# Optimization experiments

Measured on AMD Instinct MI355X. Metric: run time of the kernel, lower is better.

Reference implementation:

```python
import jax, jax.numpy as jnp
import numpy as np

N = 100_000          # nodes
E = 3_200_000        # train edges (avg degree 32)
E_TEST = 500_000     # pos/neg test edges each
F_IN, F_HID, F_OUT = 256, 16, 64


def setup_inputs() -> dict:
    key = jax.random.key(0)
    ks = jax.random.split(key, 7)
    x = jax.random.normal(ks[0], (N, F_IN), jnp.float32)
    train_edge_index = jax.random.randint(ks[1], (2, E), 0, N, dtype=jnp.int32)
    test_pos_edge_index = jax.random.randint(ks[2], (2, E_TEST), 0, N, dtype=jnp.int32)
    test_neg_edge_index = jax.random.randint(ks[3], (2, E_TEST), 0, N, dtype=jnp.int32)
    W1 = jax.random.normal(ks[4], (F_IN, F_HID), jnp.float32) / np.float32(np.sqrt(F_IN))
    b1 = jnp.zeros((F_HID,), jnp.float32)
    W2 = jax.random.normal(ks[5], (F_HID, F_OUT), jnp.float32) / np.float32(np.sqrt(F_HID))
    b2 = jnp.zeros((F_OUT,), jnp.float32)
    return dict(x=x, train_edge_index=train_edge_index,
                test_pos_edge_index=test_pos_edge_index,
                test_neg_edge_index=test_neg_edge_index,
                W1=W1, b1=b1, W2=W2, b2=b2)


def gcn_conv(x, edge_index, W, b, n):
    """PyG GCNConv: x' = D^-1/2 (A+I) D^-1/2 (x W) + b (self-loops added)."""
    h = x @ W                                  # project first (PyG order)
    loop = jnp.arange(n, dtype=edge_index.dtype)
    src = jnp.concatenate([edge_index[0], loop])
    dst = jnp.concatenate([edge_index[1], loop])
    deg = jax.ops.segment_sum(jnp.ones_like(dst, dtype=h.dtype), dst, num_segments=n)
    dinv = jnp.where(deg > 0, jax.lax.rsqrt(deg), 0.0)
    norm = dinv[src] * dinv[dst]               # per-edge symmetric norm
    msg = h[src] * norm[:, None]               # gather + scale
    out = jax.ops.segment_sum(msg, dst, num_segments=n)  # scatter-add
    return out + b


def reference(x, train_edge_index, test_pos_edge_index, test_neg_edge_index,
              W1, b1, W2, b2):
    n = x.shape[0]
    z = gcn_conv(x, train_edge_index, W1, b1, n)
    z = jax.nn.relu(z)
    z = gcn_conv(z, train_edge_index, W2, b2, n)
    edge_index = jnp.concatenate([test_pos_edge_index, test_neg_edge_index], axis=-1)
    logits = jnp.sum(z[edge_index[0]] * z[edge_index[1]], axis=-1)
    return logits
```

## Files before the change

### kernel.cpp

```cpp
#include <hip/hip_runtime.h>
#include <hip/hip_fp16.h>


#define NB_SHIFT 8
#define CAP   9728
#define CHUNK 8192

__global__ void seedprep_kernel(int* __restrict__ gtail, int nb1,
                                const float* __restrict__ W2, const float* __restrict__ b2,
                                float* __restrict__ mw) {
    int t = threadIdx.x;
    for (int i = t; i < nb1; i += 256) gtail[i] = i * CAP;
    int r = t >> 4, cc = t & 15;
    float s = 0.0f;
    for (int j = 0; j < 64; ++j) s += W2[r * 64 + j] * W2[cc * 64 + j];
    mw[t] = s;
    if (t < 16) {
        float w = 0.0f;
        for (int j = 0; j < 64; ++j) w += W2[t * 64 + j] * b2[j];
        mw[256 + t] = w;
    }
    if (t == 0) {
        float bbv = 0.0f;
        for (int j = 0; j < 64; ++j) bbv += b2[j] * b2[j];
        mw[272] = bbv;
    }
}

__global__ void __launch_bounds__(512)
passA1_kernel(const int* __restrict__ src, const int* __restrict__ dst, int E,
              int* __restrict__ gtail, unsigned* __restrict__ tmp, int nb1) {
    __shared__ int h[512];
    __shared__ int loff[512];
    __shared__ int cur[512];
    __shared__ int base[512];
    __shared__ unsigned srec[CHUNK];
    __shared__ unsigned short sbkt[CHUNK];
    int t = threadIdx.x;
    int c0 = blockIdx.x * CHUNK;
    int ce = min(CHUNK, E - c0);

    h[t] = 0;
    __syncthreads();
    for (int i = t; i < ce; i += 512)
        atomicAdd(&h[dst[c0 + i] >> NB_SHIFT], 1);
    __syncthreads();
    int cnt = h[t];
    loff[t] = cnt;
    __syncthreads();
    for (int off = 1; off < 512; off <<= 1) {
        int v = loff[t];
        int a = (t >= off) ? loff[t - off] : 0;
        __syncthreads();
        loff[t] = v + a;
        __syncthreads();
    }
    int excl = loff[t] - cnt;
    if (t < nb1) base[t] = atomicAdd(&gtail[t], cnt);
    loff[t] = excl;
    cur[t]  = excl;
    __syncthreads();
    for (int i = t; i < ce; i += 512) {
        int d = dst[c0 + i];
        int s = src[c0 + i];
        int b = d >> NB_SHIFT;
        int p = atomicAdd(&cur[b], 1);
        srec[p] = (unsigned)s | ((unsigned)(d & 255) << 20);
        sbkt[p] = (unsigned short)b;
    }
    __syncthreads();
    for (int i = t; i < ce; i += 512) {
        int b = sbkt[i];
        tmp[base[b] + (i - loff[b])] = srec[i];
    }
}

__global__ void __launch_bounds__(512)
fill2_kernel(const int* __restrict__ gtail, const unsigned* __restrict__ tmp,
             int* __restrict__ eidx, int* __restrict__ rowptr,
             int* __restrict__ counts, float* __restrict__ dinv, int n) {
    __shared__ int hh[256];
    __shared__ int sc[256];
    __shared__ int cur[256];
    __shared__ int sout[CAP];
    int b = blockIdx.x;
    int t = threadIdx.x;
    int beg = b * CAP;
    int cnt_total = gtail[b] - beg;

    if (t < 256) hh[t] = 0;
    __syncthreads();
    for (int i = t; i < cnt_total; i += 512)
        atomicAdd(&hh[tmp[beg + i] >> 20], 1);
    __syncthreads();
    if (t < 256) sc[t] = hh[t];
    __syncthreads();
    for (int off = 1; off < 256; off <<= 1) {
        int v = 0, a = 0;
        if (t < 256) { v = sc[t]; a = (t >= off) ? sc[t - off] : 0; }
        __syncthreads();
        if (t < 256) sc[t] = v + a;
        __syncthreads();
    }
    if (t < 256) {
        int ex = sc[t] - hh[t];
        cur[t] = ex;
        int v = (b << NB_SHIFT) + t;
        if (v < n) {
            rowptr[v] = beg + ex;
            counts[v] = hh[t];
            dinv[v]   = rsqrtf((float)hh[t] + 1.0f);
        }
    }
    __syncthreads();
    for (int i = t; i < cnt_total; i += 512) {
        unsigned r = tmp[beg + i];
        int p = atomicAdd(&cur[r >> 20], 1);
        sout[p] = (int)(r & 0xFFFFF);
    }
    __syncthreads();
    for (int i = t; i < cnt_total; i += 512)
        eidx[beg + i] = sout[i];
}

__global__ void __launch_bounds__(64)
gemm1_kernel(const float* __restrict__ x, const float* __restrict__ W1,
             const float* __restrict__ dinv, __half* __restrict__ hs, int n) {
    int row = blockIdx.x * 64 + threadIdx.x;
    if (row >= n) return;
    const float4* x4 = (const float4*)(x + (size_t)row * 256);
    const float4* W14 = (const float4*)W1;
    float4 a0 = {0,0,0,0}, a1 = {0,0,0,0}, a2 = {0,0,0,0}, a3 = {0,0,0,0};
    float4 buf[8];
    #pragma unroll
    for (int j = 0; j < 8; ++j) buf[j] = x4[j];
    for (int k8 = 0; k8 < 8; ++k8) {
        float4 cur[8];
        #pragma unroll
        for (int j = 0; j < 8; ++j) cur[j] = buf[j];
        if (k8 < 7) {
            #pragma unroll
            for (int j = 0; j < 8; ++j) buf[j] = x4[(k8 + 1) * 8 + j];
        }
        #pragma unroll
        for (int jj = 0; jj < 8; ++jj) {
            float4 xv = cur[jj];
            int k4 = k8 * 8 + jj;
            #pragma unroll
            for (int j = 0; j < 4; ++j) {
                float xk = (j == 0) ? xv.x : (j == 1) ? xv.y : (j == 2) ? xv.z : xv.w;
                int k = (k4 << 2) + j;
                float4 w0 = W14[k * 4 + 0];
                float4 w1 = W14[k * 4 + 1];
                float4 w2 = W14[k * 4 + 2];
                float4 w3 = W14[k * 4 + 3];
                a0.x += xk * w0.x; a0.y += xk * w0.y; a0.z += xk * w0.z; a0.w += xk * w0.w;
                a1.x += xk * w1.x; a1.y += xk * w1.y; a1.z += xk * w1.z; a1.w += xk * w1.w;
                a2.x += xk * w2.x; a2.y += xk * w2.y; a2.z += xk * w2.z; a2.w += xk * w2.w;
                a3.x += xk * w3.x; a3.y += xk * w3.y; a3.z += xk * w3.z; a3.w += xk * w3.w;
            }
        }
    }
    float di = dinv[row];
    union { __half2 h2[8]; uint4 u4[2]; } pk;
    pk.h2[0] = __floats2half2_rn(a0.x * di, a0.y * di);
    pk.h2[1] = __floats2half2_rn(a0.z * di, a0.w * di);
    pk.h2[2] = __floats2half2_rn(a1.x * di, a1.y * di);
    pk.h2[3] = __floats2half2_rn(a1.z * di, a1.w * di);
    pk.h2[4] = __floats2half2_rn(a2.x * di, a2.y * di);
    pk.h2[5] = __floats2half2_rn(a2.z * di, a2.w * di);
    pk.h2[6] = __floats2half2_rn(a3.x * di, a3.y * di);
    pk.h2[7] = __floats2half2_rn(a3.z * di, a3.w * di);
    uint4* o = (uint4*)(hs + (size_t)row * 16);
    o[0] = pk.u4[0];
    o[1] = pk.u4[1];
}

__global__ void agg1_kernel(const int* __restrict__ rowptr, const int* __restrict__ counts,
                            const int* __restrict__ eidx, const __half* __restrict__ hsh,
                            const float* __restrict__ dinv, const float* __restrict__ b1,
                            float4* __restrict__ gs4, int n) {
    const uint2* h2p = (const uint2*)hsh;
    int t = blockIdx.x * blockDim.x + threadIdx.x;
    int v = t >> 3;
    if (v >= n) return;
    int q = t & 3, hh = (t >> 2) & 1;
    int start = rowptr[v], cnt = counts[v];
    float4 s = {0, 0, 0, 0};
    int i = hh;
    for (; i + 6 < cnt; i += 8) {
        int s0 = eidx[start + i];
        int s1 = eidx[start + i + 2];
        int s2 = eidx[start + i + 4];
        int s3 = eidx[start + i + 6];
        uint2 r0 = h2p[(size_t)s0 * 4 + q];
        uint2 r1 = h2p[(size_t)s1 * 4 + q];
        uint2 r2 = h2p[(size_t)s2 * 4 + q];
        uint2 r3 = h2p[(size_t)s3 * 4 + q];
        float2 f0a = __half22float2(*(__half2*)&r0.x), f0b = __half22float2(*(__half2*)&r0.y);
        float2 f1a = __half22float2(*(__half2*)&r1.x), f1b = __half22float2(*(__half2*)&r1.y);
        float2 f2a = __half22float2(*(__half2*)&r2.x), f2b = __half22float2(*(__half2*)&r2.y);
        float2 f3a = __half22float2(*(__half2*)&r3.x), f3b = __half22float2(*(__half2*)&r3.y);
        s.x += f0a.x + f1a.x + f2a.x + f3a.x;
        s.y += f0a.y + f1a.y + f2a.y + f3a.y;
        s.z += f0b.x + f1b.x + f2b.x + f3b.x;
        s.w += f0b.y + f1b.y + f2b.y + f3b.y;
    }
    for (; i < cnt; i += 2) {
        uint2 r0 = h2p[(size_t)eidx[start + i] * 4 + q];
        float2 fa = __half22float2(*(__half2*)&r0.x), fb = __half22float2(*(__half2*)&r0.y);
        s.x += fa.x; s.y += fa.y; s.z += fb.x; s.w += fb.y;
    }
    s.x += __shfl_xor(s.x, 4);
    s.y += __shfl_xor(s.y, 4);
    s.z += __shfl_xor(s.z, 4);
    s.w += __shfl_xor(s.w, 4);
    if (hh == 0) {
        float di = dinv[v];
        uint2 rv = h2p[(size_t)v * 4 + q];
        float2 ha = __half22float2(*(__half2*)&rv.x), hb = __half22float2(*(__half2*)&rv.y);
        float4 b = ((const float4*)b1)[q];
        float4 z;
        z.x = fmaxf(di * (s.x + ha.x) + b.x, 0.0f) * di;
        z.y = fmaxf(di * (s.y + ha.y) + b.y, 0.0f) * di;
        z.z = fmaxf(di * (s.z + hb.x) + b.z, 0.0f) * di;
        z.w = fmaxf(di * (s.w + hb.y) + b.w, 0.0f) * di;
        gs4[(size_t)v * 4 + q] = z;
    }
}

__global__ void agg2y_kernel(const int* __restrict__ rowptr, const int* __restrict__ counts,
                             const int* __restrict__ eidx, const float4* __restrict__ gs4,
                             const float* __restrict__ dinv, const float* __restrict__ mw,
                             float4* __restrict__ u4, float* __restrict__ y,
                             float* __restrict__ c, int n) {
    __shared__ float su[32 * 16];
    __shared__ float sM[256];
    __shared__ float sw[16];
    int t = threadIdx.x;
    sM[t] = mw[t];
    if (t < 16) sw[t] = mw[256 + t];

    int j = t >> 3, q = t & 3, hh = (t >> 2) & 1;
    int v = blockIdx.x * 32 + j;
    if (v < n) {
        int start = rowptr[v], cnt = counts[v];
        float4 s = {0, 0, 0, 0};
        int i = hh;
        for (; i + 6 < cnt; i += 8) {
            int s0 = eidx[start + i];
            int s1 = eidx[start + i + 2];
            int s2 = eidx[start + i + 4];
            int s3 = eidx[start + i + 6];
            float4 g0 = gs4[(size_t)s0 * 4 + q];
            float4 g1 = gs4[(size_t)s1 * 4 + q];
            float4 g2 = gs4[(size_t)s2 * 4 + q];
            float4 g3 = gs4[(size_t)s3 * 4 + q];
            s.x += g0.x + g1.x + g2.x + g3.x;
            s.y += g0.y + g1.y + g2.y + g3.y;
            s.z += g0.z + g1.z + g2.z + g3.z;
            s.w += g0.w + g1.w + g2.w + g3.w;
        }
        for (; i < cnt; i += 2) {
            float4 g0 = gs4[(size_t)eidx[start + i] * 4 + q];
            s.x += g0.x; s.y += g0.y; s.z += g0.z; s.w += g0.w;
        }
        s.x += __shfl_xor(s.x, 4);
        s.y += __shfl_xor(s.y, 4);
        s.z += __shfl_xor(s.z, 4);
        s.w += __shfl_xor(s.w, 4);
        if (hh == 0) {
            float di = dinv[v];
            float4 g = gs4[(size_t)v * 4 + q];
            float4 uu;
            uu.x = di * (s.x + g.x);
            uu.y = di * (s.y + g.y);
            uu.z = di * (s.z + g.z);
            uu.w = di * (s.w + g.w);
            float* up = &su[j * 16 + q * 4];
            up[0] = uu.x; up[1] = uu.y; up[2] = uu.z; up[3] = uu.w;
            u4[(size_t)v * 4 + q] = uu;
        }
    }
    __syncthreads();
    if (v < n) {
        int l8 = t & 7;
        const float* uu = &su[j * 16];
        int c0 = l8 * 2;
        float y0 = sw[c0], y1 = sw[c0 + 1];
        #pragma unroll
        for (int k = 0; k < 16; ++k) {
            float uk = uu[k];
            y0 += uk * sM[k * 16 + c0];
            y1 += uk * sM[k * 16 + c0 + 1];
        }
        float2* yp = (float2*)(y + (size_t)v * 16 + c0);
        *yp = make_float2(y0, y1);
        if (l8 == 0) {
            float cv = 0.0f;
            #pragma unroll
            for (int k = 0; k < 16; ++k) cv += uu[k] * sw[k];
            c[v] = cv;
        }
    }
}

__global__ void edge_dot_kernel(const int* __restrict__ pa, const int* __restrict__ pb,
                                const int* __restrict__ na, const int* __restrict__ nb_,
                                int ET, const float* __restrict__ u, const float* __restrict__ y,
                                const float* __restrict__ c, const float* __restrict__ mw,
                                float* __restrict__ out) {
    int t = blockIdx.x * blockDim.x + threadIdx.x;
    int p = t >> 4, l = t & 15;
    if (p >= ET) return;
    int a0 = pa[p], b0 = pb[p];
    int a1 = na[p], b1 = nb_[p];
    float ya0 = y[(size_t)a0 * 16 + l];
    float ub0 = u[(size_t)b0 * 16 + l];
    float ya1 = y[(size_t)a1 * 16 + l];
    float ub1 = u[(size_t)b1 * 16 + l];
    float p0 = ya0 * ub0;
    float p1 = ya1 * ub1;
    p0 += __shfl_xor(p0, 1);  p1 += __shfl_xor(p1, 1);
    p0 += __shfl_xor(p0, 2);  p1 += __shfl_xor(p1, 2);
    p0 += __shfl_xor(p0, 4);  p1 += __shfl_xor(p1, 4);
    p0 += __shfl_xor(p0, 8);  p1 += __shfl_xor(p1, 8);
    if (l == 0) {
        float bb = mw[272];
        out[p]      = p0 + c[a0] + bb;
        out[ET + p] = p1 + c[a1] + bb;
    }
}

extern "C" void kernel_launch(void* const* d_in, const int* in_sizes, int n_in,
                              void* d_out, int out_size, void* d_ws, size_t ws_size,
                              hipStream_t stream) {
    const float* x    = (const float*)d_in[0];
    const int*   tei  = (const int*)d_in[1];
    const int*   tpos = (const int*)d_in[2];
    const int*   tneg = (const int*)d_in[3];
    const float* W1   = (const float*)d_in[4];
    const float* b1   = (const float*)d_in[5];
    const float* W2   = (const float*)d_in[6];
    const float* b2   = (const float*)d_in[7];
    float* out = (float*)d_out;

    int n   = in_sizes[0] / 256;
    int E   = in_sizes[1] / 2;
    int ET  = in_sizes[2] / 2;
    int nb1 = (n + 255) >> NB_SHIFT;

    char* w = (char*)d_ws;
    int*   gtail  = (int*)w;        w += 512 * 4;
    float* mw     = (float*)w;      w += 512 * 4;
    int*   rowptr = (int*)w;        w += (size_t)n * 4;
    int*   counts = (int*)w;        w += (size_t)n * 4;
    float* dinv   = (float*)w;      w += (size_t)n * 4;
    __half* hs    = (__half*)w;     w += (size_t)16 * n * 2;
    float* gs     = (float*)w;      w += (size_t)16 * n * 4;
    float* u      = (float*)w;      w += (size_t)16 * n * 4;
    float* y      = (float*)w;      w += (size_t)16 * n * 4;
    float* c      = (float*)w;      w += (size_t)n * 4;
    int*   eidx   = (int*)w;        w += (size_t)nb1 * CAP * 4;
    unsigned* tmp = (unsigned*)w;   w += (size_t)nb1 * CAP * 4;

    const int* src = tei;
    const int* dst = tei + E;

    seedprep_kernel<<<1, 256, 0, stream>>>(gtail, nb1, W2, b2, mw);
    passA1_kernel<<<(E + CHUNK - 1) / CHUNK, 512, 0, stream>>>(src, dst, E, gtail, tmp, nb1);
    fill2_kernel<<<nb1, 512, 0, stream>>>(gtail, tmp, eidx, rowptr, counts, dinv, n);

    gemm1_kernel<<<(n + 63) / 64, 64, 0, stream>>>(x, W1, dinv, hs, n);
    agg1_kernel<<<(8 * n + 255) / 256, 256, 0, stream>>>(rowptr, counts, eidx,
                                                         hs, dinv, b1,
                                                         (float4*)gs, n);
    agg2y_kernel<<<(n + 31) / 32, 256, 0, stream>>>(rowptr, counts, eidx,
                                                    (const float4*)gs, dinv, mw,
                                                    (float4*)u, y, c, n);
    edge_dot_kernel<<<(16 * ET + 255) / 256, 256, 0, stream>>>(tpos, tpos + ET, tneg, tneg + ET,
                                                               ET, u, y, c, mw, out);
}
```

Measured before the change: 338.8 us.

## Store layer-1 activations as fp16 and widen gathers to 16-byte loads

```diff
diff --git a/kernel.cpp b/kernel.cpp
--- a/kernel.cpp
+++ b/kernel.cpp
@@ -5,6 +5,15 @@
 #define NB_SHIFT 8
 #define CAP   9728
 #define CHUNK 8192
+
+__device__ __forceinline__ void acc8(float* s, uint4 r) {
+    float2 f0 = __half22float2(*(__half2*)&r.x);
+    float2 f1 = __half22float2(*(__half2*)&r.y);
+    float2 f2 = __half22float2(*(__half2*)&r.z);
+    float2 f3 = __half22float2(*(__half2*)&r.w);
+    s[0] += f0.x; s[1] += f0.y; s[2] += f1.x; s[3] += f1.y;
+    s[4] += f2.x; s[5] += f2.y; s[6] += f3.x; s[7] += f3.y;
+}
 
 __global__ void seedprep_kernel(int* __restrict__ gtail, int nb1,
                                 const float* __restrict__ W2, const float* __restrict__ b2,
@@ -179,107 +188,109 @@
 __global__ void agg1_kernel(const int* __restrict__ rowptr, const int* __restrict__ counts,
                             const int* __restrict__ eidx, const __half* __restrict__ hsh,
                             const float* __restrict__ dinv, const float* __restrict__ b1,
-                            float4* __restrict__ gs4, int n) {
-    const uint2* h2p = (const uint2*)hsh;
+                            __half* __restrict__ gsh, int n) {
+    const uint4* h4p = (const uint4*)hsh;
     int t = blockIdx.x * blockDim.x + threadIdx.x;
     int v = t >> 3;
     if (v >= n) return;
-    int q = t & 3, hh = (t >> 2) & 1;
+    int f = t & 1, e = (t >> 1) & 3;
     int start = rowptr[v], cnt = counts[v];
-    float4 s = {0, 0, 0, 0};
-    int i = hh;
-    for (; i + 6 < cnt; i += 8) {
+    float s[8] = {0, 0, 0, 0, 0, 0, 0, 0};
+    int i = e;
+    for (; i + 12 < cnt; i += 16) {
         int s0 = eidx[start + i];
-        int s1 = eidx[start + i + 2];
-        int s2 = eidx[start + i + 4];
-        int s3 = eidx[start + i + 6];
-        uint2 r0 = h2p[(size_t)s0 * 4 + q];
-        uint2 r1 = h2p[(size_t)s1 * 4 + q];
-        uint2 r2 = h2p[(size_t)s2 * 4 + q];
-        uint2 r3 = h2p[(size_t)s3 * 4 + q];
-        float2 f0a = __half22float2(*(__half2*)&r0.x), f0b = __half22float2(*(__half2*)&r0.y);
-        float2 f1a = __half22float2(*(__half2*)&r1.x), f1b = __half22float2(*(__half2*)&r1.y);
-        float2 f2a = __half22float2(*(__half2*)&r2.x), f2b = __half22float2(*(__half2*)&r2.y);
-        float2 f3a = __half22float2(*(__half2*)&r3.x), f3b = __half22float2(*(__half2*)&r3.y);
-        s.x += f0a.x + f1a.x + f2a.x + f3a.x;
-        s.y += f0a.y + f1a.y + f2a.y + f3a.y;
-        s.z += f0b.x + f1b.x + f2b.x + f3b.x;
-        s.w += f0b.y + f1b.y + f2b.y + f3b.y;
-    }
-    for (; i < cnt; i += 2) {
-        uint2 r0 = h2p[(size_t)eidx[start + i] * 4 + q];
-        float2 fa = __half22float2(*(__half2*)&r0.x), fb = __half22float2(*(__half2*)&r0.y);
-        s.x += fa.x; s.y += fa.y; s.z += fb.x; s.w += fb.y;
-    }
-    s.x += __shfl_xor(s.x, 4);
-    s.y += __shfl_xor(s.y, 4);
-    s.z += __shfl_xor(s.z, 4);
-    s.w += __shfl_xor(s.w, 4);
-    if (hh == 0) {
+        int s1 = eidx[start + i + 4];
+        int s2 = eidx[start + i + 8];
+        int s3 = eidx[start + i + 12];
+        uint4 r0 = h4p[(size_t)s0 * 2 + f];
+        uint4 r1 = h4p[(size_t)s1 * 2 + f];
+        uint4 r2 = h4p[(size_t)s2 * 2 + f];
+        uint4 r3 = h4p[(size_t)s3 * 2 + f];
+        acc8(s, r0); acc8(s, r1); acc8(s, r2); acc8(s, r3);
+    }
+    for (; i < cnt; i += 4) {
+        uint4 r0 = h4p[(size_t)eidx[start + i] * 2 + f];
+        acc8(s, r0);
+    }
+    #pragma unroll
+    for (int m = 0; m < 8; ++m) {
+        s[m] += __shfl_xor(s[m], 2);
+        s[m] += __shfl_xor(s[m], 4);
+    }
+    if (e == 0) {
         float di = dinv[v];
-        uint2 rv = h2p[(size_t)v * 4 + q];
-        float2 ha = __half22float2(*(__half2*)&rv.x), hb = __half22float2(*(__half2*)&rv.y);
-        float4 b = ((const float4*)b1)[q];
-        float4 z;
-        z.x = fmaxf(di * (s.x + ha.x) + b.x, 0.0f) * di;
-        z.y = fmaxf(di * (s.y + ha.y) + b.y, 0.0f) * di;
-        z.z = fmaxf(di * (s.z + hb.x) + b.z, 0.0f) * di;
-        z.w = fmaxf(di * (s.w + hb.y) + b.w, 0.0f) * di;
-        gs4[(size_t)v * 4 + q] = z;
+        float h[8] = {0, 0, 0, 0, 0, 0, 0, 0};
+        uint4 rv = h4p[(size_t)v * 2 + f];
+        acc8(h, rv);
+        float4 ba = ((const float4*)b1)[f * 2];
+        float4 bb = ((const float4*)b1)[f * 2 + 1];
+        float bv[8] = {ba.x, ba.y, ba.z, ba.w, bb.x, bb.y, bb.z, bb.w};
+        float z[8];
+        #pragma unroll
+        for (int m = 0; m < 8; ++m)
+            z[m] = fmaxf(di * (s[m] + h[m]) + bv[m], 0.0f) * di;
+        union { __half2 h2[4]; uint4 u4; } pk;
+        #pragma unroll
+        for (int m = 0; m < 4; ++m)
+            pk.h2[m] = __floats2half2_rn(z[2 * m], z[2 * m + 1]);
+        ((uint4*)gsh)[(size_t)v * 2 + f] = pk.u4;
     }
 }
 
 __global__ void agg2y_kernel(const int* __restrict__ rowptr, const int* __restrict__ counts,
-                             const int* __restrict__ eidx, const float4* __restrict__ gs4,
+                             const int* __restrict__ eidx, const __half* __restrict__ gsh,
                              const float* __restrict__ dinv, const float* __restrict__ mw,
                              float4* __restrict__ u4, float* __restrict__ y,
                              float* __restrict__ c, int n) {
     __shared__ float su[32 * 16];
     __shared__ float sM[256];
     __shared__ float sw[16];
+    const uint4* g4p = (const uint4*)gsh;
     int t = threadIdx.x;
     sM[t] = mw[t];
     if (t < 16) sw[t] = mw[256 + t];
 
-    int j = t >> 3, q = t & 3, hh = (t >> 2) & 1;
+    int j = t >> 3, f = t & 1, e = (t >> 1) & 3;
     int v = blockIdx.x * 32 + j;
     if (v < n) {
         int start = rowptr[v], cnt = counts[v];
-        float4 s = {0, 0, 0, 0};
-        int i = hh;
-        for (; i + 6 < cnt; i += 8) {
+        float s[8] = {0, 0, 0, 0, 0, 0, 0, 0};
+        int i = e;
+        for (; i + 12 < cnt; i += 16) {
             int s0 = eidx[start + i];
-            int s1 = eidx[start + i + 2];
-            int s2 = eidx[start + i + 4];
-            int s3 = eidx[start + i + 6];
-            float4 g0 = gs4[(size_t)s0 * 4 + q];
-            float4 g1 = gs4[(size_t)s1 * 4 + q];
-            float4 g2 = gs4[(size_t)s2 * 4 + q];
-            float4 g3 = gs4[(size_t)s3 * 4 + q];
-            s.x += g0.x + g1.x + g2.x + g3.x;
-            s.y += g0.y + g1.y + g2.y + g3.y;
-            s.z += g0.z + g1.z + g2.z + g3.z;
-            s.w += g0.w + g1.w + g2.w + g3.w;
-        }
-        for (; i < cnt; i += 2) {
-            float4 g0 = gs4[(size_t)eidx[start + i] * 4 + q];
-            s.x += g0.x; s.y += g0.y; s.z += g0.z; s.w += g0.w;
-        }
-        s.x += __shfl_xor(s.x, 4);
-        s.y += __shfl_xor(s.y, 4);
-        s.z += __shfl_xor(s.z, 4);
-        s.w += __shfl_xor(s.w, 4);
-        if (hh == 0) {
+            int s1 = eidx[start + i + 4];
+            int s2 = eidx[start + i + 8];
+            int s3 = eidx[start + i + 12];
+            uint4 r0 = g4p[(size_t)s0 * 2 + f];
+            uint4 r1 = g4p[(size_t)s1 * 2 + f];
+            uint4 r2 = g4p[(size_t)s2 * 2 + f];
+            uint4 r3 = g4p[(size_t)s3 * 2 + f];
+            acc8(s, r0); acc8(s, r1); acc8(s, r2); acc8(s, r3);
+        }
+        for (; i < cnt; i += 4) {
+            uint4 r0 = g4p[(size_t)eidx[start + i] * 2 + f];
+            acc8(s, r0);
+        }
+        #pragma unroll
+        for (int m = 0; m < 8; ++m) {
+            s[m] += __shfl_xor(s[m], 2);
+            s[m] += __shfl_xor(s[m], 4);
+        }
+        if (e == 0) {
             float di = dinv[v];
-            float4 g = gs4[(size_t)v * 4 + q];
-            float4 uu;
-            uu.x = di * (s.x + g.x);
-            uu.y = di * (s.y + g.y);
-            uu.z = di * (s.z + g.z);
-            uu.w = di * (s.w + g.w);
-            float* up = &su[j * 16 + q * 4];
-            up[0] = uu.x; up[1] = uu.y; up[2] = uu.z; up[3] = uu.w;
-            u4[(size_t)v * 4 + q] = uu;
+            float g[8] = {0, 0, 0, 0, 0, 0, 0, 0};
+            uint4 gv = g4p[(size_t)v * 2 + f];
+            acc8(g, gv);
+            float uu[8];
+            #pragma unroll
+            for (int m = 0; m < 8; ++m) uu[m] = di * (s[m] + g[m]);
+            float* up = &su[j * 16 + f * 8];
+            #pragma unroll
+            for (int m = 0; m < 8; ++m) up[m] = uu[m];
+            float4 ua = make_float4(uu[0], uu[1], uu[2], uu[3]);
+            float4 ub = make_float4(uu[4], uu[5], uu[6], uu[7]);
+            u4[(size_t)v * 4 + f * 2]     = ua;
+            u4[(size_t)v * 4 + f * 2 + 1] = ub;
         }
     }
     __syncthreads();
@@ -357,7 +368,7 @@
     int*   counts = (int*)w;        w += (size_t)n * 4;
     float* dinv   = (float*)w;      w += (size_t)n * 4;
     __half* hs    = (__half*)w;     w += (size_t)16 * n * 2;
-    float* gs     = (float*)w;      w += (size_t)16 * n * 4;
+    __half* gs    = (__half*)w;     w += (size_t)16 * n * 2;
     float* u      = (float*)w;      w += (size_t)16 * n * 4;
     float* y      = (float*)w;      w += (size_t)16 * n * 4;
     float* c      = (float*)w;      w += (size_t)n * 4;
@@ -373,10 +384,9 @@
 
     gemm1_kernel<<<(n + 63) / 64, 64, 0, stream>>>(x, W1, dinv, hs, n);
     agg1_kernel<<<(8 * n + 255) / 256, 256, 0, stream>>>(rowptr, counts, eidx,
-                                                         hs, dinv, b1,
-                                                         (float4*)gs, n);
+                                                         hs, dinv, b1, gs, n);
     agg2y_kernel<<<(n + 31) / 32, 256, 0, stream>>>(rowptr, counts, eidx,
-                                                    (const float4*)gs, dinv, mw,
+                                                    gs, dinv, mw,
                                                     (float4*)u, y, c, n);
     edge_dot_kernel<<<(16 * ET + 255) / 256, 256, 0, stream>>>(tpos, tpos + ET, tneg, tneg + ET,
                                                                ET, u, y, c, mw, out);
```

New measurement: 325.3 us. 4.0% less time.
